# Optimization experiments

Measured on AMD Instinct MI355X. Metric: run time of the kernel, lower is better.

Reference implementation:

```python
import jax, jax.numpy as jnp
import numpy as np

D_MODEL = 1024
NHEAD = 16
HEAD_DIM = D_MODEL // NHEAD
B, T = 4, 2048


def setup_inputs() -> dict:
    key = jax.random.key(0)
    ks = jax.random.split(key, 5)
    s = 0.02
    return {
        "x": jax.random.normal(ks[0], (B, T, D_MODEL), dtype=jnp.float32),
        "w_qkv": jax.random.normal(ks[1], (D_MODEL, 3 * D_MODEL), dtype=jnp.float32) * s,
        "b_qkv": jnp.zeros((3 * D_MODEL,), dtype=jnp.float32),
        "w_proj": jax.random.normal(ks[2], (D_MODEL, D_MODEL), dtype=jnp.float32) * s,
        "b_proj": jnp.zeros((D_MODEL,), dtype=jnp.float32),
    }


def reference(x, w_qkv, b_qkv, w_proj, b_proj):
    Bx, Tx, D = x.shape
    qkv = x @ w_qkv + b_qkv                      # [B,T,3D]
    qkv = qkv.reshape(Bx, Tx, 3, NHEAD, HEAD_DIM)
    q, k, v = qkv[:, :, 0], qkv[:, :, 1], qkv[:, :, 2]   # [B,T,H,hd]
    q = q.transpose(0, 2, 1, 3)                  # [B,H,T,hd]
    k = k.transpose(0, 2, 1, 3)
    v = v.transpose(0, 2, 1, 3)
    scale = 1.0 / jnp.sqrt(jnp.asarray(HEAD_DIM, dtype=x.dtype))
    attn = jnp.einsum("bhqd,bhkd->bhqk", q, k) * scale   # [B,H,T,T]
    causal = jnp.tril(jnp.ones((Tx, Tx), dtype=bool))
    attn = jnp.where(causal[None, None], attn, jnp.asarray(-jnp.inf, dtype=attn.dtype))
    attn = jax.nn.softmax(attn, axis=-1)
    # dropout p=0.0 (eval / identity)
    out = jnp.einsum("bhqk,bhkd->bhqd", attn, v)          # [B,H,T,hd]
    out = out.transpose(0, 2, 1, 3).reshape(Bx, Tx, D)
    return out @ w_proj + b_proj
```

## Files before the change

kernel.cpp:

```cpp
#include <hip/hip_runtime.h>
#include <hip/hip_bf16.h>
#include <math.h>

#define D_MODEL 1024
#define NH      16
#define HD      64
#define T_SEQ   2048
#define B_SZ    4
#define M_ROWS  (B_SZ * T_SEQ)
#define N_QKV   (3 * D_MODEL)

typedef __bf16 bf16x8 __attribute__((ext_vector_type(8)));
typedef __bf16 bf16x4 __attribute__((ext_vector_type(4)));
typedef float  f32x4  __attribute__((ext_vector_type(4)));

__device__ __forceinline__ bf16x8 cvt8(float4 a, float4 b) {
    bf16x8 v;
    v[0]=(__bf16)a.x; v[1]=(__bf16)a.y; v[2]=(__bf16)a.z; v[3]=(__bf16)a.w;
    v[4]=(__bf16)b.x; v[5]=(__bf16)b.y; v[6]=(__bf16)b.z; v[7]=(__bf16)b.w;
    return v;
}

__device__ __forceinline__ void gload_lds16(const __bf16* g, __bf16* l) {
    __builtin_amdgcn_global_load_lds(
        (const __attribute__((address_space(1))) void*)g,
        (__attribute__((address_space(3))) void*)l, 16, 0, 0);
}

__device__ __forceinline__ float exp2v(float x) {
    float r;
    asm("v_exp_f32 %0, %1" : "=v"(r) : "v"(x));
    return r;
}

__global__ __launch_bounds__(256) void cvt_bf16(const float* __restrict__ in,
                                                __bf16* __restrict__ out, int n8)
{
    int i = blockIdx.x * 256 + threadIdx.x;
    if (i < n8) {
        float4 a = ((const float4*)in)[2 * i];
        float4 b = ((const float4*)in)[2 * i + 1];
        ((bf16x8*)out)[i] = cvt8(a, b);
    }
}

__global__ __launch_bounds__(256) void transpose_cvt(
    const float* __restrict__ W, __bf16* __restrict__ WT, int R, int C)
{
    __shared__ float t[32][33];
    const int tr0 = blockIdx.y * 32, tc0 = blockIdx.x * 32;
    const int lr = threadIdx.x >> 5, lc = threadIdx.x & 31;
    #pragma unroll
    for (int i = 0; i < 4; ++i)
        t[lr + i * 8][lc] = W[(size_t)(tr0 + lr + i * 8) * C + tc0 + lc];
    __syncthreads();
    #pragma unroll
    for (int i = 0; i < 4; ++i)
        WT[(size_t)(tc0 + lr + i * 8) * R + tr0 + lc] = (__bf16)t[lc][lr + i * 8];
}

template<int MODE>
__global__ __launch_bounds__(256) void gemm_mfma(
    const __bf16* __restrict__ A, const __bf16* __restrict__ BT,
    const float* __restrict__ bias, void* __restrict__ C0,
    __bf16* __restrict__ vT, int M, int N, int K)
{
    __shared__ __bf16 As[128 * 64];
    __shared__ __bf16 Bs[128 * 64];

    const int nbn = N >> 7;
    const int nwg = gridDim.x;
    int bid = blockIdx.x;
    bid = (bid & 7) * (nwg >> 3) + (bid >> 3);
    const int tm = bid / nbn, tn = bid % nbn;
    const int row0 = tm << 7, col0 = tn << 7;

    const int tid  = threadIdx.x;
    const int wid  = tid >> 6, lane = tid & 63;
    const int wm   = wid >> 1, wn = wid & 1;
    const int g    = lane >> 4, r16 = lane & 15;

    f32x4 acc[4][4] = {};

    for (int k0 = 0; k0 < K; k0 += 64) {
        #pragma unroll
        for (int i = 0; i < 4; ++i) {
            const int seg = wid * 4 + i;
            const int row = seg * 8 + (lane >> 3);
            const int kel = ((lane & 7) * 8) ^ ((row & 7) * 8);
            gload_lds16(A  + (size_t)(row0 + row) * K + k0 + kel, As + seg * 512);
            gload_lds16(BT + (size_t)(col0 + row) * K + k0 + kel, Bs + seg * 512);
        }
        __syncthreads();

        #pragma unroll
        for (int kk = 0; kk < 2; ++kk) {
            bf16x8 af[4], bfr[4];
            #pragma unroll
            for (int mt = 0; mt < 4; ++mt) {
                const int row = wm * 64 + mt * 16 + r16;
                af[mt] = *(const bf16x8*)((const char*)As + row * 128
                             + ((kk * 64 + g * 16) ^ ((row & 7) << 4)));
            }
            #pragma unroll
            for (int nt = 0; nt < 4; ++nt) {
                const int row = wn * 64 + nt * 16 + r16;
                bfr[nt] = *(const bf16x8*)((const char*)Bs + row * 128
                             + ((kk * 64 + g * 16) ^ ((row & 7) << 4)));
            }
            #pragma unroll
            for (int mt = 0; mt < 4; ++mt)
                #pragma unroll
                for (int nt = 0; nt < 4; ++nt)
                    acc[mt][nt] = __builtin_amdgcn_mfma_f32_16x16x32_bf16(
                        af[mt], bfr[nt], acc[mt][nt], 0, 0, 0);
        }
        __syncthreads();
    }

    const bool isV = (MODE == 1) && (tn >= 16);

    #pragma unroll
    for (int mt = 0; mt < 4; ++mt) {
        #pragma unroll
        for (int nt = 0; nt < 4; ++nt) {
            const int col = col0 + wn * 64 + nt * 16 + r16;
            const float bv = bias[col];
            const int rowb = row0 + wm * 64 + mt * 16 + g * 4;
            if (MODE == 0) {
                #pragma unroll
                for (int j = 0; j < 4; ++j)
                    ((float*)C0)[(size_t)(rowb + j) * N + col] = acc[mt][nt][j] + bv;
            } else if (!isV) {
                #pragma unroll
                for (int j = 0; j < 4; ++j)
                    ((__bf16*)C0)[(size_t)(rowb + j) * 2048 + col] =
                        (__bf16)(acc[mt][nt][j] + bv);
            } else {
                const int hh = (col - 2048) >> 6, dd = (col - 2048) & 63;
                const int bb = rowb >> 11, tt = rowb & 2047;
                __bf16 p4[4];
                #pragma unroll
                for (int j = 0; j < 4; ++j) p4[j] = (__bf16)(acc[mt][nt][j] + bv);
                *(bf16x4*)&vT[((size_t)((bb * NH + hh) * HD + dd)) * T_SEQ + tt]
                    = *(const bf16x4*)p4;
            }
        }
    }
}

__global__ __launch_bounds__(256) void attn_mfma(
    const __bf16* __restrict__ qkb, const __bf16* __restrict__ vT,
    __bf16* __restrict__ aout)
{
    const int idx  = blockIdx.x;
    const int slot = idx >> 6;
    const int j    = slot & 3, p = slot >> 2;
    const int qt   = (p == 0) ? 15 - j : (p == 1) ? 8 + j : (p == 2) ? 4 + j : 3 - j;
    const int bh   = idx & 63;
    const int b    = bh >> 4;
    const int h    = bh & 15;
    const int tid  = threadIdx.x;
    const int wid  = tid >> 6;
    const int lane = tid & 63;
    const int g    = lane >> 4;
    const int n    = lane & 15;
    const int swzn = (n & 7) << 4;

    const int q0    = qt * 128;
    const int qbase = q0 + wid * 32;
    const int nkt   = 2 * qt + 2;

    __shared__ __align__(16) char Ks[64 * 128];
    __shared__ __align__(16) char Vs[64 * 128];
    __shared__ __align__(16) char Ps[4][32 * 128];

    const int srow = tid >> 2;
    const int sb0  = (tid & 3) << 4;
    const int swzw = (srow & 7) << 4;
    const int sd8  = (tid & 3) * 8;

    const float qscale = 0.125f * 1.44269504089f;
    bf16x8 qa[2][2];
    #pragma unroll
    for (int rb = 0; rb < 2; ++rb) {
        const size_t qrow = (size_t)(b * T_SEQ + qbase + rb * 16 + n) * 2048
                            + (size_t)h * HD;
        qa[rb][0] = *(const bf16x8*)&qkb[qrow + g * 8];
        qa[rb][1] = *(const bf16x8*)&qkb[qrow + 32 + g * 8];
        #pragma unroll
        for (int jj = 0; jj < 8; ++jj) {
            qa[rb][0][jj] = (__bf16)((float)qa[rb][0][jj] * qscale);
            qa[rb][1][jj] = (__bf16)((float)qa[rb][1][jj] * qscale);
        }
    }

    f32x4 o[2][4] = {};
    float mrow[2][4] = {};
    float lrow[2][4] = {};

    const __bf16* gK = qkb + (size_t)(b * T_SEQ + srow) * 2048 + 1024
                       + (size_t)h * HD + sd8;
    const __bf16* gV = vT + ((size_t)((b * NH + h) * HD + srow)) * T_SEQ + sd8;

    bf16x8 kreg0 = *(const bf16x8*)gK;
    bf16x8 kreg1 = *(const bf16x8*)(gK + 32);
    bf16x8 vreg0 = *(const bf16x8*)gV;
    bf16x8 vreg1 = *(const bf16x8*)(gV + 32);

    for (int kt = 0; kt < nkt; ++kt) {
        *(bf16x8*)(Ks + srow * 128 + (sb0 ^ swzw))        = kreg0;
        *(bf16x8*)(Ks + srow * 128 + ((sb0 + 64) ^ swzw)) = kreg1;
        *(bf16x8*)(Vs + srow * 128 + (sb0 ^ swzw))        = vreg0;
        *(bf16x8*)(Vs + srow * 128 + ((sb0 + 64) ^ swzw)) = vreg1;
        __syncthreads();

        if (kt + 1 < nkt) {
            const size_t kb2 = (size_t)(kt + 1) * 64;
            kreg0 = *(const bf16x8*)(gK + kb2 * 2048);
            kreg1 = *(const bf16x8*)(gK + kb2 * 2048 + 32);
            vreg0 = *(const bf16x8*)(gV + kb2);
            vreg1 = *(const bf16x8*)(gV + kb2 + 32);
        }

        const int kb0 = kt * 64;
        const bool active = (kb0 <= qbase + 31);

        if (active) {
            f32x4 s4[2][4] = {};
            __builtin_amdgcn_s_setprio(1);
            #pragma unroll
            for (int cc = 0; cc < 2; ++cc) {
                bf16x8 kf[4];
                #pragma unroll
                for (int sub = 0; sub < 4; ++sub)
                    kf[sub] = *(const bf16x8*)(Ks + (sub * 16 + n) * 128
                                               + ((cc * 64 + g * 16) ^ swzn));
                #pragma unroll
                for (int rb = 0; rb < 2; ++rb)
                    #pragma unroll
                    for (int sub = 0; sub < 4; ++sub)
                        s4[rb][sub] = __builtin_amdgcn_mfma_f32_16x16x32_bf16(
                            qa[rb][cc], kf[sub], s4[rb][sub], 0, 0, 0);
            }
            __builtin_amdgcn_s_setprio(0);

            const bool needmask = (kb0 + 63 > qbase);

            #pragma unroll
            for (int rb = 0; rb < 2; ++rb) {
                if (needmask) {
                    #pragma unroll
                    for (int r = 0; r < 4; ++r) {
                        const int qrow = qbase + rb * 16 + 4 * g + r;
                        #pragma unroll
                        for (int sub = 0; sub < 4; ++sub)
                            if (kb0 + sub * 16 + n > qrow) s4[rb][sub][r] = -INFINITY;
                    }
                }
                float pm[4];
                int ok = 1;
                #pragma unroll
                for (int r = 0; r < 4; ++r) {
                    pm[r] = fmaxf(fmaxf(s4[rb][0][r], s4[rb][1][r]),
                                  fmaxf(s4[rb][2][r], s4[rb][3][r]));
                    ok &= (pm[r] <= mrow[rb][r] + 8.f);
                }
                if (__all(ok)) {
                    #pragma unroll
                    for (int r = 0; r < 4; ++r) {
                        const float m = mrow[rb][r];
                        const float p0 = exp2v(s4[rb][0][r] - m);
                        const float p1 = exp2v(s4[rb][1][r] - m);
                        const float p2 = exp2v(s4[rb][2][r] - m);
                        const float p3 = exp2v(s4[rb][3][r] - m);
                        lrow[rb][r] += (p0 + p1) + (p2 + p3);
                        char* prow = Ps[wid] + (rb * 16 + 4 * g + r) * 128;
                        const int pswz = ((4 * g + r) & 7) << 4;
                        *(__bf16*)(prow + ((2 * n)      ^ pswz)) = (__bf16)p0;
                        *(__bf16*)(prow + ((2 * n + 32) ^ pswz)) = (__bf16)p1;
                        *(__bf16*)(prow + ((2 * n + 64) ^ pswz)) = (__bf16)p2;
                        *(__bf16*)(prow + ((2 * n + 96) ^ pswz)) = (__bf16)p3;
                    }
                } else {
                    #pragma unroll
                    for (int r = 0; r < 4; ++r) {
                        float tm = pm[r];
                        #pragma unroll
                        for (int off = 1; off < 16; off <<= 1)
                            tm = fmaxf(tm, __shfl_xor(tm, off));
                        const float mnew = fmaxf(mrow[rb][r], tm);
                        const float corr = exp2v(mrow[rb][r] - mnew);
                        mrow[rb][r] = mnew;
                        const float p0 = exp2v(s4[rb][0][r] - mnew);
                        const float p1 = exp2v(s4[rb][1][r] - mnew);
                        const float p2 = exp2v(s4[rb][2][r] - mnew);
                        const float p3 = exp2v(s4[rb][3][r] - mnew);
                        lrow[rb][r] = lrow[rb][r] * corr + (p0 + p1) + (p2 + p3);
                        #pragma unroll
                        for (int nt = 0; nt < 4; ++nt) o[rb][nt][r] *= corr;
                        char* prow = Ps[wid] + (rb * 16 + 4 * g + r) * 128;
                        const int pswz = ((4 * g + r) & 7) << 4;
                        *(__bf16*)(prow + ((2 * n)      ^ pswz)) = (__bf16)p0;
                        *(__bf16*)(prow + ((2 * n + 32) ^ pswz)) = (__bf16)p1;
                        *(__bf16*)(prow + ((2 * n + 64) ^ pswz)) = (__bf16)p2;
                        *(__bf16*)(prow + ((2 * n + 96) ^ pswz)) = (__bf16)p3;
                    }
                }
            }

            __builtin_amdgcn_s_setprio(1);
            #pragma unroll
            for (int cc = 0; cc < 2; ++cc) {
                bf16x8 vf[4];
                #pragma unroll
                for (int nt = 0; nt < 4; ++nt)
                    vf[nt] = *(const bf16x8*)(Vs + (nt * 16 + n) * 128
                                              + ((cc * 64 + g * 16) ^ swzn));
                #pragma unroll
                for (int rb = 0; rb < 2; ++rb) {
                    bf16x8 pa = *(const bf16x8*)(Ps[wid] + (rb * 16 + n) * 128
                                                 + ((cc * 64 + g * 16) ^ swzn));
                    #pragma unroll
                    for (int nt = 0; nt < 4; ++nt)
                        o[rb][nt] = __builtin_amdgcn_mfma_f32_16x16x32_bf16(
                            pa, vf[nt], o[rb][nt], 0, 0, 0);
                }
            }
            __builtin_amdgcn_s_setprio(0);
        }
        __syncthreads();
    }

    #pragma unroll
    for (int rb = 0; rb < 2; ++rb) {
        float inv[4];
        #pragma unroll
        for (int r = 0; r < 4; ++r) {
            float s = lrow[rb][r];
            #pragma unroll
            for (int off = 1; off < 16; off <<= 1)
                s += __shfl_xor(s, off);
            inv[r] = 1.f / s;
        }
        const size_t obase = (size_t)(b * T_SEQ + qbase + rb * 16) * D_MODEL
                             + (size_t)h * HD;
        #pragma unroll
        for (int nt = 0; nt < 4; ++nt)
            #pragma unroll
            for (int r = 0; r < 4; ++r)
                aout[obase + (size_t)(4 * g + r) * D_MODEL + nt * 16 + n]
                    = (__bf16)(o[rb][nt][r] * inv[r]);
    }
}

extern "C" void kernel_launch(void* const* d_in, const int* in_sizes, int n_in,
                              void* d_out, int out_size, void* d_ws, size_t ws_size,
                              hipStream_t stream)
{
    const float* x      = (const float*)d_in[0];
    const float* w_qkv  = (const float*)d_in[1];
    const float* b_qkv  = (const float*)d_in[2];
    const float* w_proj = (const float*)d_in[3];
    const float* b_proj = (const float*)d_in[4];
    float* out = (float*)d_out;

    char* ws = (char*)d_ws;
    __bf16* qkb    = (__bf16*)ws;
    __bf16* vTb    = qkb + (size_t)M_ROWS * 2048;
    __bf16* xb     = vTb + (size_t)NH * B_SZ * HD * T_SEQ;
    __bf16* wqkvT  = xb + (size_t)M_ROWS * D_MODEL;
    __bf16* wprojT = wqkvT + (size_t)N_QKV * D_MODEL;
    __bf16* aout   = wprojT + (size_t)D_MODEL * D_MODEL;

    cvt_bf16<<<dim3(M_ROWS * D_MODEL / 8 / 256), 256, 0, stream>>>(
        x, xb, M_ROWS * D_MODEL / 8);
    transpose_cvt<<<dim3(N_QKV / 32, D_MODEL / 32), 256, 0, stream>>>(
        w_qkv, wqkvT, D_MODEL, N_QKV);
    transpose_cvt<<<dim3(D_MODEL / 32, D_MODEL / 32), 256, 0, stream>>>(
        w_proj, wprojT, D_MODEL, D_MODEL);

    gemm_mfma<1><<<dim3((M_ROWS / 128) * (N_QKV / 128)), 256, 0, stream>>>(
        xb, wqkvT, b_qkv, qkb, vTb, M_ROWS, N_QKV, D_MODEL);

    attn_mfma<<<dim3(B_SZ * NH * 16), 256, 0, stream>>>(qkb, vTb, aout);

    gemm_mfma<0><<<dim3((M_ROWS / 128) * (D_MODEL / 128)), 256, 0, stream>>>(
        aout, wprojT, b_proj, out, nullptr, M_ROWS, D_MODEL, D_MODEL);
}
```

Before: 193.3 us.

## Shrink attention query tile to 64 rows with 2-wave blocks

The attention kernel now uses 64-query blocks of two waves instead of 128-query blocks of four, doubling the grid and using a new heavy/light interleaved tile order for load balance. Every wave's key range now matches its block, so the per-wave 'active' check and the idle waves on the diagonal tile go away. Each thread stages more K/V chunks per tile. In exchange, each K/V tile loaded into LDS is reused by fewer query rows, raising global and LDS load traffic per unit of compute.

After: 203.7 us. +5.4%, slower.

```diff
diff --git a/kernel.cpp b/kernel.cpp
--- a/kernel.cpp
+++ b/kernel.cpp
@@ -149,14 +149,14 @@
     }
 }
 
-__global__ __launch_bounds__(256) void attn_mfma(
+__global__ __launch_bounds__(128) void attn_mfma(
     const __bf16* __restrict__ qkb, const __bf16* __restrict__ vT,
     __bf16* __restrict__ aout)
 {
     const int idx  = blockIdx.x;
-    const int slot = idx >> 6;
-    const int j    = slot & 3, p = slot >> 2;
-    const int qt   = (p == 0) ? 15 - j : (p == 1) ? 8 + j : (p == 2) ? 4 + j : 3 - j;
+    const int s    = idx >> 6;
+    const int qt   = (s & 4) ? ((s >> 3) * 4 + (s & 3))
+                             : (31 - (s >> 3) * 4 - (s & 3));
     const int bh   = idx & 63;
     const int b    = bh >> 4;
     const int h    = bh & 15;
@@ -167,18 +167,17 @@
     const int n    = lane & 15;
     const int swzn = (n & 7) << 4;
 
-    const int q0    = qt * 128;
+    const int q0    = qt * 64;
     const int qbase = q0 + wid * 32;
-    const int nkt   = 2 * qt + 2;
+    const int nkt   = qt + 1;
 
     __shared__ __align__(16) char Ks[64 * 128];
     __shared__ __align__(16) char Vs[64 * 128];
-    __shared__ __align__(16) char Ps[4][32 * 128];
-
-    const int srow = tid >> 2;
-    const int sb0  = (tid & 3) << 4;
+    __shared__ __align__(16) char Ps[2][32 * 128];
+
+    const int srow = tid >> 1;
+    const int sch2 = tid & 1;
     const int swzw = (srow & 7) << 4;
-    const int sd8  = (tid & 3) * 8;
 
     const float qscale = 0.125f * 1.44269504089f;
     bf16x8 qa[2][2];
@@ -200,135 +199,137 @@
     float lrow[2][4] = {};
 
     const __bf16* gK = qkb + (size_t)(b * T_SEQ + srow) * 2048 + 1024
-                       + (size_t)h * HD + sd8;
-    const __bf16* gV = vT + ((size_t)((b * NH + h) * HD + srow)) * T_SEQ + sd8;
-
-    bf16x8 kreg0 = *(const bf16x8*)gK;
-    bf16x8 kreg1 = *(const bf16x8*)(gK + 32);
-    bf16x8 vreg0 = *(const bf16x8*)gV;
-    bf16x8 vreg1 = *(const bf16x8*)(gV + 32);
+                       + (size_t)h * HD + sch2 * 32;
+    const __bf16* gV = vT + ((size_t)((b * NH + h) * HD + srow)) * T_SEQ + sch2 * 32;
+
+    bf16x8 kreg[4], vreg[4];
+    #pragma unroll
+    for (int c = 0; c < 4; ++c) {
+        kreg[c] = *(const bf16x8*)(gK + c * 8);
+        vreg[c] = *(const bf16x8*)(gV + c * 8);
+    }
 
     for (int kt = 0; kt < nkt; ++kt) {
-        *(bf16x8*)(Ks + srow * 128 + (sb0 ^ swzw))        = kreg0;
-        *(bf16x8*)(Ks + srow * 128 + ((sb0 + 64) ^ swzw)) = kreg1;
-        *(bf16x8*)(Vs + srow * 128 + (sb0 ^ swzw))        = vreg0;
-        *(bf16x8*)(Vs + srow * 128 + ((sb0 + 64) ^ swzw)) = vreg1;
+        #pragma unroll
+        for (int c = 0; c < 4; ++c) {
+            const int boff = (sch2 * 64 + c * 16) ^ swzw;
+            *(bf16x8*)(Ks + srow * 128 + boff) = kreg[c];
+            *(bf16x8*)(Vs + srow * 128 + boff) = vreg[c];
+        }
         __syncthreads();
 
         if (kt + 1 < nkt) {
             const size_t kb2 = (size_t)(kt + 1) * 64;
-            kreg0 = *(const bf16x8*)(gK + kb2 * 2048);
-            kreg1 = *(const bf16x8*)(gK + kb2 * 2048 + 32);
-            vreg0 = *(const bf16x8*)(gV + kb2);
-            vreg1 = *(const bf16x8*)(gV + kb2 + 32);
+            #pragma unroll
+            for (int c = 0; c < 4; ++c) {
+                kreg[c] = *(const bf16x8*)(gK + kb2 * 2048 + c * 8);
+                vreg[c] = *(const bf16x8*)(gV + kb2 + c * 8);
+            }
         }
 
         const int kb0 = kt * 64;
-        const bool active = (kb0 <= qbase + 31);
-
-        if (active) {
-            f32x4 s4[2][4] = {};
-            __builtin_amdgcn_s_setprio(1);
-            #pragma unroll
-            for (int cc = 0; cc < 2; ++cc) {
-                bf16x8 kf[4];
+
+        f32x4 s4[2][4] = {};
+        __builtin_amdgcn_s_setprio(1);
+        #pragma unroll
+        for (int cc = 0; cc < 2; ++cc) {
+            bf16x8 kf[4];
+            #pragma unroll
+            for (int sub = 0; sub < 4; ++sub)
+                kf[sub] = *(const bf16x8*)(Ks + (sub * 16 + n) * 128
+                                           + ((cc * 64 + g * 16) ^ swzn));
+            #pragma unroll
+            for (int rb = 0; rb < 2; ++rb)
                 #pragma unroll
                 for (int sub = 0; sub < 4; ++sub)
-                    kf[sub] = *(const bf16x8*)(Ks + (sub * 16 + n) * 128
-                                               + ((cc * 64 + g * 16) ^ swzn));
-                #pragma unroll
-                for (int rb = 0; rb < 2; ++rb)
+                    s4[rb][sub] = __builtin_amdgcn_mfma_f32_16x16x32_bf16(
+                        qa[rb][cc], kf[sub], s4[rb][sub], 0, 0, 0);
+        }
+        __builtin_amdgcn_s_setprio(0);
+
+        const bool needmask = (kb0 + 63 > qbase);
+
+        #pragma unroll
+        for (int rb = 0; rb < 2; ++rb) {
+            if (needmask) {
+                #pragma unroll
+                for (int r = 0; r < 4; ++r) {
+                    const int qrow = qbase + rb * 16 + 4 * g + r;
                     #pragma unroll
                     for (int sub = 0; sub < 4; ++sub)
-                        s4[rb][sub] = __builtin_amdgcn_mfma_f32_16x16x32_bf16(
-                            qa[rb][cc], kf[sub], s4[rb][sub], 0, 0, 0);
-            }
-            __builtin_amdgcn_s_setprio(0);
-
-            const bool needmask = (kb0 + 63 > qbase);
-
+                        if (kb0 + sub * 16 + n > qrow) s4[rb][sub][r] = -INFINITY;
+                }
+            }
+            float pm[4];
+            int ok = 1;
+            #pragma unroll
+            for (int r = 0; r < 4; ++r) {
+                pm[r] = fmaxf(fmaxf(s4[rb][0][r], s4[rb][1][r]),
+                              fmaxf(s4[rb][2][r], s4[rb][3][r]));
+                ok &= (pm[r] <= mrow[rb][r] + 8.f);
+            }
+            if (__all(ok)) {
+                #pragma unroll
+                for (int r = 0; r < 4; ++r) {
+                    const float m = mrow[rb][r];
+                    const float p0 = exp2v(s4[rb][0][r] - m);
+                    const float p1 = exp2v(s4[rb][1][r] - m);
+                    const float p2 = exp2v(s4[rb][2][r] - m);
+                    const float p3 = exp2v(s4[rb][3][r] - m);
+                    lrow[rb][r] += (p0 + p1) + (p2 + p3);
+                    char* prow = Ps[wid] + (rb * 16 + 4 * g + r) * 128;
+                    const int pswz = ((4 * g + r) & 7) << 4;
+                    *(__bf16*)(prow + ((2 * n)      ^ pswz)) = (__bf16)p0;
+                    *(__bf16*)(prow + ((2 * n + 32) ^ pswz)) = (__bf16)p1;
+                    *(__bf16*)(prow + ((2 * n + 64) ^ pswz)) = (__bf16)p2;
+                    *(__bf16*)(prow + ((2 * n + 96) ^ pswz)) = (__bf16)p3;
+                }
+            } else {
+                #pragma unroll
+                for (int r = 0; r < 4; ++r) {
+                    float tm = pm[r];
+                    #pragma unroll
+                    for (int off = 1; off < 16; off <<= 1)
+                        tm = fmaxf(tm, __shfl_xor(tm, off));
+                    const float mnew = fmaxf(mrow[rb][r], tm);
+                    const float corr = exp2v(mrow[rb][r] - mnew);
+                    mrow[rb][r] = mnew;
+                    const float p0 = exp2v(s4[rb][0][r] - mnew);
+                    const float p1 = exp2v(s4[rb][1][r] - mnew);
+                    const float p2 = exp2v(s4[rb][2][r] - mnew);
+                    const float p3 = exp2v(s4[rb][3][r] - mnew);
+                    lrow[rb][r] = lrow[rb][r] * corr + (p0 + p1) + (p2 + p3);
+                    #pragma unroll
+                    for (int nt = 0; nt < 4; ++nt) o[rb][nt][r] *= corr;
+                    char* prow = Ps[wid] + (rb * 16 + 4 * g + r) * 128;
+                    const int pswz = ((4 * g + r) & 7) << 4;
+                    *(__bf16*)(prow + ((2 * n)      ^ pswz)) = (__bf16)p0;
+                    *(__bf16*)(prow + ((2 * n + 32) ^ pswz)) = (__bf16)p1;
+                    *(__bf16*)(prow + ((2 * n + 64) ^ pswz)) = (__bf16)p2;
+                    *(__bf16*)(prow + ((2 * n + 96) ^ pswz)) = (__bf16)p3;
+                }
+            }
+        }
+
+        __builtin_amdgcn_s_setprio(1);
+        #pragma unroll
+        for (int cc = 0; cc < 2; ++cc) {
+            bf16x8 vf[4];
+            #pragma unroll
+            for (int nt = 0; nt < 4; ++nt)
+                vf[nt] = *(const bf16x8*)(Vs + (nt * 16 + n) * 128
+                                          + ((cc * 64 + g * 16) ^ swzn));
             #pragma unroll
             for (int rb = 0; rb < 2; ++rb) {
-                if (needmask) {
-                    #pragma unroll
-                    for (int r = 0; r < 4; ++r) {
-                        const int qrow = qbase + rb * 16 + 4 * g + r;
-                        #pragma unroll
-                        for (int sub = 0; sub < 4; ++sub)
-                            if (kb0 + sub * 16 + n > qrow) s4[rb][sub][r] = -INFINITY;
-                    }
-                }
-                float pm[4];
-                int ok = 1;
-                #pragma unroll
-                for (int r = 0; r < 4; ++r) {
-                    pm[r] = fmaxf(fmaxf(s4[rb][0][r], s4[rb][1][r]),
-                                  fmaxf(s4[rb][2][r], s4[rb][3][r]));
-                    ok &= (pm[r] <= mrow[rb][r] + 8.f);
-                }
-                if (__all(ok)) {
-                    #pragma unroll
-                    for (int r = 0; r < 4; ++r) {
-                        const float m = mrow[rb][r];
-                        const float p0 = exp2v(s4[rb][0][r] - m);
-                        const float p1 = exp2v(s4[rb][1][r] - m);
-                        const float p2 = exp2v(s4[rb][2][r] - m);
-                        const float p3 = exp2v(s4[rb][3][r] - m);
-                        lrow[rb][r] += (p0 + p1) + (p2 + p3);
-                        char* prow = Ps[wid] + (rb * 16 + 4 * g + r) * 128;
-                        const int pswz = ((4 * g + r) & 7) << 4;
-                        *(__bf16*)(prow + ((2 * n)      ^ pswz)) = (__bf16)p0;
-                        *(__bf16*)(prow + ((2 * n + 32) ^ pswz)) = (__bf16)p1;
-                        *(__bf16*)(prow + ((2 * n + 64) ^ pswz)) = (__bf16)p2;
-                        *(__bf16*)(prow + ((2 * n + 96) ^ pswz)) = (__bf16)p3;
-                    }
-                } else {
-                    #pragma unroll
-                    for (int r = 0; r < 4; ++r) {
-                        float tm = pm[r];
-                        #pragma unroll
-                        for (int off = 1; off < 16; off <<= 1)
-                            tm = fmaxf(tm, __shfl_xor(tm, off));
-                        const float mnew = fmaxf(mrow[rb][r], tm);
-                        const float corr = exp2v(mrow[rb][r] - mnew);
-                        mrow[rb][r] = mnew;
-                        const float p0 = exp2v(s4[rb][0][r] - mnew);
-                        const float p1 = exp2v(s4[rb][1][r] - mnew);
-                        const float p2 = exp2v(s4[rb][2][r] - mnew);
-                        const float p3 = exp2v(s4[rb][3][r] - mnew);
-                        lrow[rb][r] = lrow[rb][r] * corr + (p0 + p1) + (p2 + p3);
-                        #pragma unroll
-                        for (int nt = 0; nt < 4; ++nt) o[rb][nt][r] *= corr;
-                        char* prow = Ps[wid] + (rb * 16 + 4 * g + r) * 128;
-                        const int pswz = ((4 * g + r) & 7) << 4;
-                        *(__bf16*)(prow + ((2 * n)      ^ pswz)) = (__bf16)p0;
-                        *(__bf16*)(prow + ((2 * n + 32) ^ pswz)) = (__bf16)p1;
-                        *(__bf16*)(prow + ((2 * n + 64) ^ pswz)) = (__bf16)p2;
-                        *(__bf16*)(prow + ((2 * n + 96) ^ pswz)) = (__bf16)p3;
-                    }
-                }
-            }
-
-            __builtin_amdgcn_s_setprio(1);
-            #pragma unroll
-            for (int cc = 0; cc < 2; ++cc) {
-                bf16x8 vf[4];
+                bf16x8 pa = *(const bf16x8*)(Ps[wid] + (rb * 16 + n) * 128
+                                             + ((cc * 64 + g * 16) ^ swzn));
                 #pragma unroll
                 for (int nt = 0; nt < 4; ++nt)
-                    vf[nt] = *(const bf16x8*)(Vs + (nt * 16 + n) * 128
-                                              + ((cc * 64 + g * 16) ^ swzn));
-                #pragma unroll
-                for (int rb = 0; rb < 2; ++rb) {
-                    bf16x8 pa = *(const bf16x8*)(Ps[wid] + (rb * 16 + n) * 128
-                                                 + ((cc * 64 + g * 16) ^ swzn));
-                    #pragma unroll
-                    for (int nt = 0; nt < 4; ++nt)
-                        o[rb][nt] = __builtin_amdgcn_mfma_f32_16x16x32_bf16(
-                            pa, vf[nt], o[rb][nt], 0, 0, 0);
-                }
-            }
-            __builtin_amdgcn_s_setprio(0);
-        }
+                    o[rb][nt] = __builtin_amdgcn_mfma_f32_16x16x32_bf16(
+                        pa, vf[nt], o[rb][nt], 0, 0, 0);
+            }
+        }
+        __builtin_amdgcn_s_setprio(0);
         __syncthreads();
     }
 
@@ -337,11 +338,11 @@
         float inv[4];
         #pragma unroll
         for (int r = 0; r < 4; ++r) {
-            float s = lrow[rb][r];
+            float ssum = lrow[rb][r];
             #pragma unroll
             for (int off = 1; off < 16; off <<= 1)
-                s += __shfl_xor(s, off);
-            inv[r] = 1.f / s;
+                ssum += __shfl_xor(ssum, off);
+            inv[r] = 1.f / ssum;
         }
         const size_t obase = (size_t)(b * T_SEQ + qbase + rb * 16) * D_MODEL
                              + (size_t)h * HD;
@@ -383,7 +384,7 @@
     gemm_mfma<1><<<dim3((M_ROWS / 128) * (N_QKV / 128)), 256, 0, stream>>>(
         xb, wqkvT, b_qkv, qkb, vTb, M_ROWS, N_QKV, D_MODEL);
 
-    attn_mfma<<<dim3(B_SZ * NH * 16), 256, 0, stream>>>(qkb, vTb, aout);
+    attn_mfma<<<dim3(B_SZ * NH * 32), 128, 0, stream>>>(qkb, vTb, aout);
 
     gemm_mfma<0><<<dim3((M_ROWS / 128) * (D_MODEL / 128)), 256, 0, stream>>>(
         aout, wprojT, b_proj, out, nullptr, M_ROWS, D_MODEL, D_MODEL);
```

## Load K/V fragments directly from global memory per wave, drop shared staging

Applied to the files above, without the earlier changes.

Removes the shared-memory K/V tiles and block-wide barriers. Each wave now loads its own K and V MFMA fragments straight from global memory (relying on L1/L2 for reuse) and runs only as many key tiles as its causal range needs. This removes LDS write/read traffic, two __syncthreads per tile and the idle waves past the diagonal. In exchange it quadruples global/L2 load traffic, loses software prefetch overlap, and uses strided uncoalesced K loads.

New measurement: 242.6 us. +25.5%, slower.

```diff
diff --git a/kernel.cpp b/kernel.cpp
--- a/kernel.cpp
+++ b/kernel.cpp
@@ -165,20 +165,12 @@
     const int lane = tid & 63;
     const int g    = lane >> 4;
     const int n    = lane & 15;
-    const int swzn = (n & 7) << 4;
 
     const int q0    = qt * 128;
     const int qbase = q0 + wid * 32;
-    const int nkt   = 2 * qt + 2;
-
-    __shared__ __align__(16) char Ks[64 * 128];
-    __shared__ __align__(16) char Vs[64 * 128];
+    const int nktw  = 2 * qt + 1 + (wid >> 1);
+
     __shared__ __align__(16) char Ps[4][32 * 128];
-
-    const int srow = tid >> 2;
-    const int sb0  = (tid & 3) << 4;
-    const int swzw = (srow & 7) << 4;
-    const int sd8  = (tid & 3) * 8;
 
     const float qscale = 0.125f * 1.44269504089f;
     bf16x8 qa[2][2];
@@ -199,137 +191,121 @@
     float mrow[2][4] = {};
     float lrow[2][4] = {};
 
-    const __bf16* gK = qkb + (size_t)(b * T_SEQ + srow) * 2048 + 1024
-                       + (size_t)h * HD + sd8;
-    const __bf16* gV = vT + ((size_t)((b * NH + h) * HD + srow)) * T_SEQ + sd8;
-
-    bf16x8 kreg0 = *(const bf16x8*)gK;
-    bf16x8 kreg1 = *(const bf16x8*)(gK + 32);
-    bf16x8 vreg0 = *(const bf16x8*)gV;
-    bf16x8 vreg1 = *(const bf16x8*)(gV + 32);
-
-    for (int kt = 0; kt < nkt; ++kt) {
-        *(bf16x8*)(Ks + srow * 128 + (sb0 ^ swzw))        = kreg0;
-        *(bf16x8*)(Ks + srow * 128 + ((sb0 + 64) ^ swzw)) = kreg1;
-        *(bf16x8*)(Vs + srow * 128 + (sb0 ^ swzw))        = vreg0;
-        *(bf16x8*)(Vs + srow * 128 + ((sb0 + 64) ^ swzw)) = vreg1;
-        __syncthreads();
-
-        if (kt + 1 < nkt) {
-            const size_t kb2 = (size_t)(kt + 1) * 64;
-            kreg0 = *(const bf16x8*)(gK + kb2 * 2048);
-            kreg1 = *(const bf16x8*)(gK + kb2 * 2048 + 32);
-            vreg0 = *(const bf16x8*)(gV + kb2);
-            vreg1 = *(const bf16x8*)(gV + kb2 + 32);
-        }
-
+    const __bf16* kbase = qkb + (size_t)b * T_SEQ * 2048 + 1024 + (size_t)h * HD
+                          + g * 8;
+    const __bf16* vbase = vT + ((size_t)((b * NH + h) * HD + n)) * T_SEQ
+                          + g * 8;
+
+    for (int kt = 0; kt < nktw; ++kt) {
         const int kb0 = kt * 64;
-        const bool active = (kb0 <= qbase + 31);
-
-        if (active) {
-            f32x4 s4[2][4] = {};
-            __builtin_amdgcn_s_setprio(1);
-            #pragma unroll
-            for (int cc = 0; cc < 2; ++cc) {
-                bf16x8 kf[4];
+
+        bf16x8 kf[2][4];
+        #pragma unroll
+        for (int cc = 0; cc < 2; ++cc)
+            #pragma unroll
+            for (int sub = 0; sub < 4; ++sub)
+                kf[cc][sub] = *(const bf16x8*)(kbase
+                    + (size_t)(kb0 + sub * 16 + n) * 2048 + cc * 32);
+
+        f32x4 s4[2][4] = {};
+        __builtin_amdgcn_s_setprio(1);
+        #pragma unroll
+        for (int cc = 0; cc < 2; ++cc)
+            #pragma unroll
+            for (int rb = 0; rb < 2; ++rb)
                 #pragma unroll
                 for (int sub = 0; sub < 4; ++sub)
-                    kf[sub] = *(const bf16x8*)(Ks + (sub * 16 + n) * 128
-                                               + ((cc * 64 + g * 16) ^ swzn));
-                #pragma unroll
-                for (int rb = 0; rb < 2; ++rb)
+                    s4[rb][sub] = __builtin_amdgcn_mfma_f32_16x16x32_bf16(
+                        qa[rb][cc], kf[cc][sub], s4[rb][sub], 0, 0, 0);
+        __builtin_amdgcn_s_setprio(0);
+
+        bf16x8 vf[2][4];
+        #pragma unroll
+        for (int cc = 0; cc < 2; ++cc)
+            #pragma unroll
+            for (int nt = 0; nt < 4; ++nt)
+                vf[cc][nt] = *(const bf16x8*)(vbase
+                    + (size_t)(nt * 16) * T_SEQ + kb0 + cc * 32);
+
+        const bool needmask = (kb0 + 63 > qbase);
+
+        #pragma unroll
+        for (int rb = 0; rb < 2; ++rb) {
+            if (needmask) {
+                #pragma unroll
+                for (int r = 0; r < 4; ++r) {
+                    const int qrow = qbase + rb * 16 + 4 * g + r;
                     #pragma unroll
                     for (int sub = 0; sub < 4; ++sub)
-                        s4[rb][sub] = __builtin_amdgcn_mfma_f32_16x16x32_bf16(
-                            qa[rb][cc], kf[sub], s4[rb][sub], 0, 0, 0);
-            }
-            __builtin_amdgcn_s_setprio(0);
-
-            const bool needmask = (kb0 + 63 > qbase);
-
+                        if (kb0 + sub * 16 + n > qrow) s4[rb][sub][r] = -INFINITY;
+                }
+            }
+            float pm[4];
+            int ok = 1;
+            #pragma unroll
+            for (int r = 0; r < 4; ++r) {
+                pm[r] = fmaxf(fmaxf(s4[rb][0][r], s4[rb][1][r]),
+                              fmaxf(s4[rb][2][r], s4[rb][3][r]));
+                ok &= (pm[r] <= mrow[rb][r] + 8.f);
+            }
+            if (__all(ok)) {
+                #pragma unroll
+                for (int r = 0; r < 4; ++r) {
+                    const float m = mrow[rb][r];
+                    const float p0 = exp2v(s4[rb][0][r] - m);
+                    const float p1 = exp2v(s4[rb][1][r] - m);
+                    const float p2 = exp2v(s4[rb][2][r] - m);
+                    const float p3 = exp2v(s4[rb][3][r] - m);
+                    lrow[rb][r] += (p0 + p1) + (p2 + p3);
+                    char* prow = Ps[wid] + (rb * 16 + 4 * g + r) * 128;
+                    const int pswz = ((4 * g + r) & 7) << 4;
+                    *(__bf16*)(prow + ((2 * n)      ^ pswz)) = (__bf16)p0;
+                    *(__bf16*)(prow + ((2 * n + 32) ^ pswz)) = (__bf16)p1;
+                    *(__bf16*)(prow + ((2 * n + 64) ^ pswz)) = (__bf16)p2;
+                    *(__bf16*)(prow + ((2 * n + 96) ^ pswz)) = (__bf16)p3;
+                }
+            } else {
+                #pragma unroll
+                for (int r = 0; r < 4; ++r) {
+                    float tm = pm[r];
+                    #pragma unroll
+                    for (int off = 1; off < 16; off <<= 1)
+                        tm = fmaxf(tm, __shfl_xor(tm, off));
+                    const float mnew = fmaxf(mrow[rb][r], tm);
+                    const float corr = exp2v(mrow[rb][r] - mnew);
+                    mrow[rb][r] = mnew;
+                    const float p0 = exp2v(s4[rb][0][r] - mnew);
+                    const float p1 = exp2v(s4[rb][1][r] - mnew);
+                    const float p2 = exp2v(s4[rb][2][r] - mnew);
+                    const float p3 = exp2v(s4[rb][3][r] - mnew);
+                    lrow[rb][r] = lrow[rb][r] * corr + (p0 + p1) + (p2 + p3);
+                    #pragma unroll
+                    for (int nt = 0; nt < 4; ++nt) o[rb][nt][r] *= corr;
+                    char* prow = Ps[wid] + (rb * 16 + 4 * g + r) * 128;
+                    const int pswz = ((4 * g + r) & 7) << 4;
+                    *(__bf16*)(prow + ((2 * n)      ^ pswz)) = (__bf16)p0;
+                    *(__bf16*)(prow + ((2 * n + 32) ^ pswz)) = (__bf16)p1;
+                    *(__bf16*)(prow + ((2 * n + 64) ^ pswz)) = (__bf16)p2;
+                    *(__bf16*)(prow + ((2 * n + 96) ^ pswz)) = (__bf16)p3;
+                }
+            }
+        }
+
+        const int swzn = (n & 7) << 4;
+        __builtin_amdgcn_s_setprio(1);
+        #pragma unroll
+        for (int cc = 0; cc < 2; ++cc) {
             #pragma unroll
             for (int rb = 0; rb < 2; ++rb) {
-                if (needmask) {
-                    #pragma unroll
-                    for (int r = 0; r < 4; ++r) {
-                        const int qrow = qbase + rb * 16 + 4 * g + r;
-                        #pragma unroll
-                        for (int sub = 0; sub < 4; ++sub)
-                            if (kb0 + sub * 16 + n > qrow) s4[rb][sub][r] = -INFINITY;
-                    }
-                }
-                float pm[4];
-                int ok = 1;
-                #pragma unroll
-                for (int r = 0; r < 4; ++r) {
-                    pm[r] = fmaxf(fmaxf(s4[rb][0][r], s4[rb][1][r]),
-                                  fmaxf(s4[rb][2][r], s4[rb][3][r]));
-                    ok &= (pm[r] <= mrow[rb][r] + 8.f);
-                }
-                if (__all(ok)) {
-                    #pragma unroll
-                    for (int r = 0; r < 4; ++r) {
-                        const float m = mrow[rb][r];
-                        const float p0 = exp2v(s4[rb][0][r] - m);
-                        const float p1 = exp2v(s4[rb][1][r] - m);
-                        const float p2 = exp2v(s4[rb][2][r] - m);
-                        const float p3 = exp2v(s4[rb][3][r] - m);
-                        lrow[rb][r] += (p0 + p1) + (p2 + p3);
-                        char* prow = Ps[wid] + (rb * 16 + 4 * g + r) * 128;
-                        const int pswz = ((4 * g + r) & 7) << 4;
-                        *(__bf16*)(prow + ((2 * n)      ^ pswz)) = (__bf16)p0;
-                        *(__bf16*)(prow + ((2 * n + 32) ^ pswz)) = (__bf16)p1;
-                        *(__bf16*)(prow + ((2 * n + 64) ^ pswz)) = (__bf16)p2;
-                        *(__bf16*)(prow + ((2 * n + 96) ^ pswz)) = (__bf16)p3;
-                    }
-                } else {
-                    #pragma unroll
-                    for (int r = 0; r < 4; ++r) {
-                        float tm = pm[r];
-                        #pragma unroll
-                        for (int off = 1; off < 16; off <<= 1)
-                            tm = fmaxf(tm, __shfl_xor(tm, off));
-                        const float mnew = fmaxf(mrow[rb][r], tm);
-                        const float corr = exp2v(mrow[rb][r] - mnew);
-                        mrow[rb][r] = mnew;
-                        const float p0 = exp2v(s4[rb][0][r] - mnew);
-                        const float p1 = exp2v(s4[rb][1][r] - mnew);
-                        const float p2 = exp2v(s4[rb][2][r] - mnew);
-                        const float p3 = exp2v(s4[rb][3][r] - mnew);
-                        lrow[rb][r] = lrow[rb][r] * corr + (p0 + p1) + (p2 + p3);
-                        #pragma unroll
-                        for (int nt = 0; nt < 4; ++nt) o[rb][nt][r] *= corr;
-                        char* prow = Ps[wid] + (rb * 16 + 4 * g + r) * 128;
-                        const int pswz = ((4 * g + r) & 7) << 4;
-                        *(__bf16*)(prow + ((2 * n)      ^ pswz)) = (__bf16)p0;
-                        *(__bf16*)(prow + ((2 * n + 32) ^ pswz)) = (__bf16)p1;
-                        *(__bf16*)(prow + ((2 * n + 64) ^ pswz)) = (__bf16)p2;
-                        *(__bf16*)(prow + ((2 * n + 96) ^ pswz)) = (__bf16)p3;
-                    }
-                }
-            }
-
-            __builtin_amdgcn_s_setprio(1);
-            #pragma unroll
-            for (int cc = 0; cc < 2; ++cc) {
-                bf16x8 vf[4];
+                bf16x8 pa = *(const bf16x8*)(Ps[wid] + (rb * 16 + n) * 128
+                                             + ((cc * 64 + g * 16) ^ swzn));
                 #pragma unroll
                 for (int nt = 0; nt < 4; ++nt)
-                    vf[nt] = *(const bf16x8*)(Vs + (nt * 16 + n) * 128
-                                              + ((cc * 64 + g * 16) ^ swzn));
-                #pragma unroll
-                for (int rb = 0; rb < 2; ++rb) {
-                    bf16x8 pa = *(const bf16x8*)(Ps[wid] + (rb * 16 + n) * 128
-                                                 + ((cc * 64 + g * 16) ^ swzn));
-                    #pragma unroll
-                    for (int nt = 0; nt < 4; ++nt)
-                        o[rb][nt] = __builtin_amdgcn_mfma_f32_16x16x32_bf16(
-                            pa, vf[nt], o[rb][nt], 0, 0, 0);
-                }
-            }
-            __builtin_amdgcn_s_setprio(0);
-        }
-        __syncthreads();
+                    o[rb][nt] = __builtin_amdgcn_mfma_f32_16x16x32_bf16(
+                        pa, vf[cc][nt], o[rb][nt], 0, 0, 0);
+            }
+        }
+        __builtin_amdgcn_s_setprio(0);
     }
 
     #pragma unroll
@@ -337,11 +313,11 @@
         float inv[4];
         #pragma unroll
         for (int r = 0; r < 4; ++r) {
-            float s = lrow[rb][r];
+            float ssum = lrow[rb][r];
             #pragma unroll
             for (int off = 1; off < 16; off <<= 1)
-                s += __shfl_xor(s, off);
-            inv[r] = 1.f / s;
+                ssum += __shfl_xor(ssum, off);
+            inv[r] = 1.f / ssum;
         }
         const size_t obase = (size_t)(b * T_SEQ + qbase + rb * 16) * D_MODEL
                              + (size_t)h * HD;
```
